# Kernel optimization log

Hardware: AMD Instinct MI355X
Metric: run time of the kernel (lower is better)

## Reference

```python
import jax, jax.numpy as jnp
import numpy as np

N_NODES = 50000
N_EDGES = 800000
IN_CH = 128
HID = 64
OUT_CH = 40


def _sage_conv(x, src, dst, W_l, b_l, W_r):
    # PyG SAGEConv (mean aggr): out = lin_l(mean_{j in N(i)} x_j) + lin_r(x_i)
    msgs = x[src]                                                # [E, d]
    summed = jax.ops.segment_sum(msgs, dst, num_segments=N_NODES)
    counts = jax.ops.segment_sum(jnp.ones((src.shape[0],), x.dtype), dst,
                                 num_segments=N_NODES)
    mean = summed / jnp.maximum(counts, 1.0)[:, None]            # [N, d]
    return mean @ W_l.T + b_l + x @ W_r.T


def setup_inputs() -> dict:
    key = jax.random.key(0)
    ks = jax.random.split(key, 8)
    x = jax.random.normal(ks[0], (N_NODES, IN_CH), dtype=jnp.float32)
    edge_index = jax.random.randint(ks[1], (2, N_EDGES), 0, N_NODES, dtype=jnp.int64)
    s1 = 1.0 / np.sqrt(IN_CH)
    s2 = 1.0 / np.sqrt(HID)
    W1_l = jax.random.uniform(ks[2], (HID, IN_CH), jnp.float32, -s1, s1)
    W1_r = jax.random.uniform(ks[3], (HID, IN_CH), jnp.float32, -s1, s1)
    b1 = jax.random.uniform(ks[4], (HID,), jnp.float32, -s1, s1)
    W2_l = jax.random.uniform(ks[5], (OUT_CH, HID), jnp.float32, -s2, s2)
    W2_r = jax.random.uniform(ks[6], (OUT_CH, HID), jnp.float32, -s2, s2)
    b2 = jax.random.uniform(ks[7], (OUT_CH,), jnp.float32, -s2, s2)
    return {"x": x, "edge_index": edge_index, "W1_l": W1_l, "b1": b1,
            "W1_r": W1_r, "W2_l": W2_l, "b2": b2, "W2_r": W2_r}


def reference(x, edge_index, W1_l, b1, W1_r, W2_l, b2, W2_r):
    src, dst = edge_index[0], edge_index[1]
    h = _sage_conv(x, src, dst, W1_l, b1, W1_r)
    h = jax.nn.relu(h)                       # dropout is identity in eval
    h = _sage_conv(h, src, dst, W2_l, b2, W2_r)
    return jax.nn.log_softmax(h, axis=-1)
```

## Files before the change

### kernel.cpp

```cpp
#include <hip/hip_runtime.h>

#define N_NODES 50000
#define N_EDGES 800000
#define IN_CH 128
#define HID 64
#define OUT_CH 40
#define BSHIFT 7
#define BNODES 128
#define NBUCKETS 391
#define NBLK 256
#define EPB 3125
#define NSEG (NBUCKETS * NBLK)
#define SCHUNK 1024
#define NSCANA ((NSEG + SCHUNK - 1) / SCHUNK)
#define MAXB 4096


typedef __attribute__((ext_vector_type(8))) short short8v;
typedef __attribute__((ext_vector_type(4))) float float4v;

__device__ __forceinline__ unsigned f2bf_u(float f) {
  unsigned u = __float_as_uint(f);
  return (u + 0x7FFF + ((u >> 16) & 1)) >> 16;
}
__device__ __forceinline__ ushort f2bf(float f) { return (ushort)f2bf_u(f); }
__device__ __forceinline__ float bf2f(ushort u) {
  return __uint_as_float(((unsigned)u) << 16);
}
__device__ __forceinline__ float bflo(unsigned u) {
  return __uint_as_float(u << 16);
}
__device__ __forceinline__ float bfhi(unsigned u) {
  return __uint_as_float(u & 0xFFFF0000u);
}

__global__ __launch_bounds__(256) void histB_kernel(const int* __restrict__ dst,
                                                    int* __restrict__ blkcnt) {
  __shared__ int h[NBUCKETS];
  for (int i = threadIdx.x; i < NBUCKETS; i += 256) h[i] = 0;
  __syncthreads();
  int blk = blockIdx.x;
  int e0 = blk * EPB, e1 = min(e0 + EPB, N_EDGES);
  for (int e = e0 + threadIdx.x; e < e1; e += 256)
    atomicAdd(&h[dst[e] >> BSHIFT], 1);
  __syncthreads();
  for (int i = threadIdx.x; i < NBUCKETS; i += 256)
    blkcnt[(i << 8) | blk] = h[i];
}

__global__ __launch_bounds__(256) void scanA_kernel(
    const int* __restrict__ blkcnt, int* __restrict__ segoff,
    int* __restrict__ asum) {
  __shared__ int s[256];
  int t = threadIdx.x;
  int idx0 = blockIdx.x * SCHUNK + t * 4;
  int v[4], tot = 0;
#pragma unroll
  for (int j = 0; j < 4; ++j) {
    int i = idx0 + j;
    v[j] = (i < NSEG) ? blkcnt[i] : 0;
    tot += v[j];
  }
  s[t] = tot;
  __syncthreads();
  for (int o = 1; o < 256; o <<= 1) {
    int u = (t >= o) ? s[t - o] : 0;
    __syncthreads();
    s[t] += u;
    __syncthreads();
  }
  int pre = s[t] - tot;
#pragma unroll
  for (int j = 0; j < 4; ++j) {
    int i = idx0 + j;
    if (i < NSEG) segoff[i] = pre;
    pre += v[j];
  }
  if (t == 255) asum[blockIdx.x] = s[255];
}

__global__ __launch_bounds__(256) void scanB_kernel(int* __restrict__ asum) {
  __shared__ int s[256];
  int t = threadIdx.x;
  int v = (t < NSCANA) ? asum[t] : 0;
  s[t] = v;
  __syncthreads();
  for (int o = 1; o < 256; o <<= 1) {
    int u = (t >= o) ? s[t - o] : 0;
    __syncthreads();
    s[t] += u;
    __syncthreads();
  }
  if (t < NSCANA) asum[t] = s[t] - v;
}

__global__ __launch_bounds__(256) void scanC_kernel(int* __restrict__ segoff,
                                                    const int* __restrict__ asum) {
  int add = asum[blockIdx.x];
  int idx0 = blockIdx.x * SCHUNK + threadIdx.x * 4;
#pragma unroll
  for (int j = 0; j < 4; ++j) {
    int i = idx0 + j;
    if (i < NSEG) segoff[i] += add;
  }
}

__global__ __launch_bounds__(256) void placeB_kernel(
    const int* __restrict__ src, const int* __restrict__ dst,
    const int* __restrict__ segoff, unsigned* __restrict__ pairbuf) {
  __shared__ int cur[NBUCKETS];
  int blk = blockIdx.x;
  for (int b = threadIdx.x; b < NBUCKETS; b += 256)
    cur[b] = segoff[(b << 8) | blk];
  __syncthreads();
  int e0 = blk * EPB, e1 = min(e0 + EPB, N_EDGES);
  for (int e = e0 + threadIdx.x; e < e1; e += 256) {
    int d = dst[e];
    int pos = atomicAdd(&cur[d >> BSHIFT], 1);
    pairbuf[pos] = ((unsigned)src[e] << BSHIFT) | (unsigned)(d & (BNODES - 1));
  }
}

__global__ __launch_bounds__(256) void placeC_kernel(
    const unsigned* __restrict__ pairbuf, const int* __restrict__ segoff,
    int* __restrict__ cnt, int* __restrict__ off, int* __restrict__ csr) {
  __shared__ int lcnt[BNODES];
  __shared__ int woff[BNODES];
  __shared__ int lcur[BNODES];
  __shared__ int sscan[256];
  __shared__ int slot[MAXB];
  int b = blockIdx.x;
  int start = segoff[b << 8];
  int end = (b == NBUCKETS - 1) ? N_EDGES : segoff[(b + 1) << 8];
  int n0 = b << BSHIFT;
  int nn = min(BNODES, N_NODES - n0);
  int len = end - start;
  for (int i = threadIdx.x; i < nn; i += 256) {
    lcnt[i] = 0;
    lcur[i] = 0;
  }
  __syncthreads();
  for (int p = start + threadIdx.x; p < end; p += 256)
    atomicAdd(&lcnt[pairbuf[p] & (BNODES - 1)], 1);
  __syncthreads();
  int v = (threadIdx.x < nn) ? lcnt[threadIdx.x] : 0;
  sscan[threadIdx.x] = v;
  __syncthreads();
  for (int o = 1; o < 256; o <<= 1) {
    int t2 = (threadIdx.x >= o) ? sscan[threadIdx.x - o] : 0;
    __syncthreads();
    sscan[threadIdx.x] += t2;
    __syncthreads();
  }
  if (threadIdx.x < nn) {
    woff[threadIdx.x] = sscan[threadIdx.x] - v;
    cnt[n0 + threadIdx.x] = v;
    off[n0 + threadIdx.x] = start + sscan[threadIdx.x] - v;
  }
  __syncthreads();
  if (len <= MAXB) {
    for (int p = start + threadIdx.x; p < end; p += 256) {
      unsigned e = pairbuf[p];
      int local = (int)(e & (BNODES - 1));
      int pos = woff[local] + atomicAdd(&lcur[local], 1);
      slot[pos] = (int)(e >> BSHIFT);
    }
    __syncthreads();
    for (int p = threadIdx.x; p < len; p += 256) csr[start + p] = slot[p];
  } else {
    for (int p = start + threadIdx.x; p < end; p += 256) {
      unsigned e = pairbuf[p];
      int local = (int)(e & (BNODES - 1));
      int pos = woff[local] + atomicAdd(&lcur[local], 1);
      csr[start + pos] = (int)(e >> BSHIFT);
    }
  }
}

__device__ __forceinline__ uint4 pack8(const float* p) {
  float4 a = *reinterpret_cast<const float4*>(p);
  float4 b = *reinterpret_cast<const float4*>(p + 4);
  uint4 r;
  r.x = f2bf_u(a.x) | (f2bf_u(a.y) << 16);
  r.y = f2bf_u(a.z) | (f2bf_u(a.w) << 16);
  r.z = f2bf_u(b.x) | (f2bf_u(b.y) << 16);
  r.w = f2bf_u(b.z) | (f2bf_u(b.w) << 16);
  return r;
}

__global__ __launch_bounds__(256) void xform1_kernel(
    const float* __restrict__ x, const float* __restrict__ W1l,
    const float* __restrict__ W1r, const float* __restrict__ b1,
    ushort* __restrict__ xwl, float* __restrict__ xwr) {
  __shared__ ushort sWl[64 * 128];
  __shared__ ushort sWr[64 * 128];
  __shared__ ushort sx[64 * 128];
  __shared__ float sb[64];

  int nblk = blockIdx.x * 64;
  for (int q = threadIdx.x; q < 1024; q += 256) {
    int row = q >> 4, c8 = (q & 15) << 3;
    int boff = row * 256 + (((c8 << 1)) ^ ((row & 15) << 4));
    int n = nblk + row;
    uint4 p = make_uint4(0, 0, 0, 0);
    if (n < N_NODES) p = pack8(x + (size_t)n * IN_CH + c8);
    *reinterpret_cast<uint4*>((char*)sx + boff) = p;
  }
  for (int q = threadIdx.x; q < 1024; q += 256) {
    int row = q >> 4, c8 = (q & 15) << 3;
    int boff = row * 256 + (((c8 << 1)) ^ ((row & 15) << 4));
    *reinterpret_cast<uint4*>((char*)sWl + boff) =
        pack8(W1l + row * IN_CH + c8);
    *reinterpret_cast<uint4*>((char*)sWr + boff) =
        pack8(W1r + row * IN_CH + c8);
  }
  if (threadIdx.x < 64) sb[threadIdx.x] = b1[threadIdx.x];
  __syncthreads();

  int wave = threadIdx.x >> 6, lane = threadIdx.x & 63;
  int nloc = lane & 15, g = lane >> 4;

  float4v accl[4], accr[4];
#pragma unroll
  for (int m = 0; m < 4; ++m) {
    accl[m] = (float4v){0.f, 0.f, 0.f, 0.f};
    accr[m] = (float4v){0.f, 0.f, 0.f, 0.f};
  }

  int xrow = wave * 16 + nloc;
#pragma unroll
  for (int kt = 0; kt < 4; ++kt) {
    int cb = kt * 64 + g * 16;
    short8v bx = *reinterpret_cast<const short8v*>(
        (char*)sx + xrow * 256 + (cb ^ ((xrow & 15) << 4)));
#pragma unroll
    for (int m = 0; m < 4; ++m) {
      int wrow = m * 16 + nloc;
      int so = wrow * 256 + (cb ^ ((wrow & 15) << 4));
      short8v al = *reinterpret_cast<const short8v*>((char*)sWl + so);
      short8v ar = *reinterpret_cast<const short8v*>((char*)sWr + so);
      accl[m] = __builtin_amdgcn_mfma_f32_16x16x32_bf16(al, bx, accl[m], 0, 0, 0);
      accr[m] = __builtin_amdgcn_mfma_f32_16x16x32_bf16(ar, bx, accr[m], 0, 0, 0);
    }
  }

  int n = nblk + wave * 16 + nloc;
  if (n < N_NODES) {
#pragma unroll
    for (int m = 0; m < 4; ++m) {
      int h0 = m * 16 + g * 4;
      uint2 pl;
      pl.x = f2bf_u(accl[m][0]) | (f2bf_u(accl[m][1]) << 16);
      pl.y = f2bf_u(accl[m][2]) | (f2bf_u(accl[m][3]) << 16);
      *reinterpret_cast<uint2*>(xwl + (size_t)n * HID + h0) = pl;
      float4 vr;
      vr.x = accr[m][0] + sb[h0 + 0];
      vr.y = accr[m][1] + sb[h0 + 1];
      vr.z = accr[m][2] + sb[h0 + 2];
      vr.w = accr[m][3] + sb[h0 + 3];
      *reinterpret_cast<float4*>(xwr + (size_t)n * HID + h0) = vr;
    }
  }
}

__global__ __launch_bounds__(256) void agg1_kernel(
    const ushort* __restrict__ xwl, const float* __restrict__ xwr,
    const int* __restrict__ cnt, const int* __restrict__ off,
    const int* __restrict__ csr, float* __restrict__ h1) {
  int wave = threadIdx.x >> 6, lane = threadIdx.x & 63;
  int n = blockIdx.x * 4 + wave;
  if (n >= N_NODES) return;

  int deg = cnt[n], base = off[n];
  int half = lane >> 5;
  int cp = lane & 31;
  float ax = 0.f, ay = 0.f;

  if (deg > 0) {
    int k = 0;
    for (; k + 16 <= deg; k += 16) {
      int e[8];
#pragma unroll
      for (int j = 0; j < 8; ++j) e[j] = csr[base + k + 2 * j + half];
      unsigned u[8];
#pragma unroll
      for (int j = 0; j < 8; ++j)
        u[j] = *reinterpret_cast<const unsigned*>(xwl + (size_t)e[j] * HID +
                                                  2 * cp);
#pragma unroll
      for (int j = 0; j < 8; ++j) {
        ax += bflo(u[j]);
        ay += bfhi(u[j]);
      }
    }
    if (k + 8 <= deg) {
      int e[4];
#pragma unroll
      for (int j = 0; j < 4; ++j) e[j] = csr[base + k + 2 * j + half];
      unsigned u[4];
#pragma unroll
      for (int j = 0; j < 4; ++j)
        u[j] = *reinterpret_cast<const unsigned*>(xwl + (size_t)e[j] * HID +
                                                  2 * cp);
#pragma unroll
      for (int j = 0; j < 4; ++j) {
        ax += bflo(u[j]);
        ay += bfhi(u[j]);
      }
      k += 8;
    }
    if (k < deg) {
#pragma unroll
      for (int j = 0; j < 4; ++j) {
        int idx = k + 2 * j + half;
        bool valid = idx < deg;
        int e = csr[base + (valid ? idx : 0)];
        unsigned u =
            *reinterpret_cast<const unsigned*>(xwl + (size_t)e * HID + 2 * cp);
        if (valid) {
          ax += bflo(u);
          ay += bfhi(u);
        }
      }
    }
    ax += __shfl_xor(ax, 32);
    ay += __shfl_xor(ay, 32);
  }

  float inv = 1.0f / fmaxf((float)deg, 1.0f);
  const float2 s =
      *reinterpret_cast<const float2*>(xwr + (size_t)n * HID + 2 * cp);
  float2 h;
  h.x = fmaxf(ax * inv + s.x, 0.f);
  h.y = fmaxf(ay * inv + s.y, 0.f);
  if (half == 0)
    *reinterpret_cast<float2*>(h1 + (size_t)n * HID + 2 * cp) = h;
}

__global__ __launch_bounds__(256) void xform2_kernel(
    const float* __restrict__ h1, const float* __restrict__ W2l,
    const float* __restrict__ W2r, const float* __restrict__ b2,
    ushort* __restrict__ hw2, float* __restrict__ self2) {
  __shared__ unsigned sWl[HID / 2][OUT_CH + 1];
  __shared__ unsigned sWr[HID / 2][OUT_CH + 1];
  __shared__ float sh[32][HID];
  for (int i = threadIdx.x; i < OUT_CH * (HID / 2); i += 256) {
    int o = i >> 5, c2 = i & 31;
    float a = W2l[o * HID + 2 * c2], b = W2l[o * HID + 2 * c2 + 1];
    sWl[c2][o] = (unsigned)f2bf(a) | ((unsigned)f2bf(b) << 16);
    float c = W2r[o * HID + 2 * c2], d = W2r[o * HID + 2 * c2 + 1];
    sWr[c2][o] = (unsigned)f2bf(c) | ((unsigned)f2bf(d) << 16);
  }
  int nblk = blockIdx.x * 32;
  for (int s = threadIdx.x; s < 32 * (HID / 4); s += 256) {
    int node = s >> 4, c4 = s & 15;
    int n = nblk + node;
    float4 v = make_float4(0.f, 0.f, 0.f, 0.f);
    if (n < N_NODES)
      v = *reinterpret_cast<const float4*>(h1 + (size_t)n * HID + c4 * 4);
    *reinterpret_cast<float4*>(&sh[node][c4 * 4]) = v;
  }
  __syncthreads();

  int wave = threadIdx.x >> 6, lane = threadIdx.x & 63;
  int n0 = nblk + wave * 8;
  if (n0 >= N_NODES || lane >= OUT_CH) return;
  float bias = b2[lane];

  float accl[8], accr[8];
#pragma unroll
  for (int i = 0; i < 8; ++i) {
    accl[i] = 0.f;
    accr[i] = bias;
  }
  const int nb = wave * 8;
  int nvalid = min(8, N_NODES - n0);
  for (int c = 0; c < HID; c += 4) {
    unsigned ul0 = sWl[(c >> 1) + 0][lane], ul1 = sWl[(c >> 1) + 1][lane];
    unsigned ur0 = sWr[(c >> 1) + 0][lane], ur1 = sWr[(c >> 1) + 1][lane];
    float wl0 = bflo(ul0), wl1 = bfhi(ul0), wl2 = bflo(ul1), wl3 = bfhi(ul1);
    float wr0 = bflo(ur0), wr1 = bfhi(ur0), wr2 = bflo(ur1), wr3 = bfhi(ur1);
#pragma unroll
    for (int i = 0; i < 8; ++i) {
      const float4 hv = *reinterpret_cast<const float4*>(&sh[nb + i][c]);
      accl[i] = fmaf(hv.x, wl0, accl[i]);
      accr[i] = fmaf(hv.x, wr0, accr[i]);
      accl[i] = fmaf(hv.y, wl1, accl[i]);
      accr[i] = fmaf(hv.y, wr1, accr[i]);
      accl[i] = fmaf(hv.z, wl2, accl[i]);
      accr[i] = fmaf(hv.z, wr2, accr[i]);
      accl[i] = fmaf(hv.w, wl3, accl[i]);
      accr[i] = fmaf(hv.w, wr3, accr[i]);
    }
  }
  for (int i = 0; i < nvalid; ++i) {
    hw2[(size_t)(n0 + i) * OUT_CH + lane] = f2bf(accl[i]);
    self2[(size_t)(n0 + i) * OUT_CH + lane] = accr[i];
  }
}

__global__ __launch_bounds__(256) void agg2_kernel(
    const ushort* __restrict__ hw2, const float* __restrict__ self2,
    const int* __restrict__ cnt, const int* __restrict__ off,
    const int* __restrict__ csr, float* __restrict__ out) {
  int wave = threadIdx.x >> 6, lane = threadIdx.x & 63;
  int n = blockIdx.x * 4 + wave;
  if (n >= N_NODES) return;

  int deg = cnt[n], base = off[n];
  float logit = -1e30f;
  if (lane < OUT_CH) {
    float acc = 0.f;
    int k = 0;
    for (; k + 16 <= deg; k += 16) {
      int e[16];
#pragma unroll
      for (int j = 0; j < 16; ++j) e[j] = csr[base + k + j];
      float v[16];
#pragma unroll
      for (int j = 0; j < 16; ++j)
        v[j] = bf2f(hw2[(size_t)e[j] * OUT_CH + lane]);
#pragma unroll
      for (int j = 0; j < 16; ++j) acc += v[j];
    }
    if (k + 8 <= deg) {
      int e[8];
#pragma unroll
      for (int j = 0; j < 8; ++j) e[j] = csr[base + k + j];
      float v[8];
#pragma unroll
      for (int j = 0; j < 8; ++j)
        v[j] = bf2f(hw2[(size_t)e[j] * OUT_CH + lane]);
#pragma unroll
      for (int j = 0; j < 8; ++j) acc += v[j];
      k += 8;
    }
    if (k < deg) {
#pragma unroll
      for (int i = 0; i < 8; ++i) {
        int kk = k + i;
        int s_ = csr[base + (kk < deg ? kk : k)];
        float v = bf2f(hw2[(size_t)s_ * OUT_CH + lane]);
        if (kk < deg) acc += v;
      }
    }
    logit = acc / fmaxf((float)deg, 1.0f) + self2[(size_t)n * OUT_CH + lane];
  }
  float m = logit;
  for (int o = 32; o; o >>= 1) m = fmaxf(m, __shfl_xor(m, o));
  float e = (lane < OUT_CH) ? expf(logit - m) : 0.f;
  float ssum = e;
  for (int o = 32; o; o >>= 1) ssum += __shfl_xor(ssum, o);
  float lse = logf(ssum);
  if (lane < OUT_CH) out[(size_t)n * OUT_CH + lane] = logit - m - lse;
}

extern "C" void kernel_launch(void* const* d_in, const int* in_sizes, int n_in,
                              void* d_out, int out_size, void* d_ws, size_t ws_size,
                              hipStream_t stream) {
  const float* x   = (const float*)d_in[0];
  const int*   ei  = (const int*)d_in[1];
  const float* W1l = (const float*)d_in[2];
  const float* b1  = (const float*)d_in[3];
  const float* W1r = (const float*)d_in[4];
  const float* W2l = (const float*)d_in[5];
  const float* b2  = (const float*)d_in[6];
  const float* W2r = (const float*)d_in[7];
  float* out = (float*)d_out;

  const int* src = ei;
  const int* dst = ei + N_EDGES;

  float* xwr        = (float*)d_ws;
  unsigned* pairbuf = (unsigned*)d_ws;
  float* self2 = xwr + (size_t)N_NODES * HID;
  float* h1    = self2 + (size_t)N_NODES * OUT_CH;
  ushort* xwl  = (ushort*)(h1 + (size_t)N_NODES * HID);
  ushort* hw2  = xwl + (size_t)N_NODES * HID;
  int* blkcnt = (int*)(hw2 + (size_t)N_NODES * OUT_CH);
  int* segoff = blkcnt + NSEG;
  int* asum   = segoff + NSEG;
  int* cnt    = asum + 256;
  int* off    = cnt + N_NODES;
  int* csr    = off + N_NODES;

  histB_kernel<<<NBLK, 256, 0, stream>>>(dst, blkcnt);
  scanA_kernel<<<NSCANA, 256, 0, stream>>>(blkcnt, segoff, asum);
  scanB_kernel<<<1, 256, 0, stream>>>(asum);
  scanC_kernel<<<NSCANA, 256, 0, stream>>>(segoff, asum);
  placeB_kernel<<<NBLK, 256, 0, stream>>>(src, dst, segoff, pairbuf);
  placeC_kernel<<<NBUCKETS, 256, 0, stream>>>(pairbuf, segoff, cnt, off, csr);

  xform1_kernel<<<(N_NODES + 63) / 64, 256, 0, stream>>>(x, W1l, W1r, b1, xwl,
                                                         xwr);
  agg1_kernel<<<(N_NODES + 3) / 4, 256, 0, stream>>>(xwl, xwr, cnt, off, csr,
                                                     h1);
  xform2_kernel<<<(N_NODES + 31) / 32, 256, 0, stream>>>(h1, W2l, W2r, b2, hw2,
                                                         self2);
  agg2_kernel<<<(N_NODES + 3) / 4, 256, 0, stream>>>(hw2, self2, cnt, off, csr,
                                                     out);
}
```

Baseline: 127.8 us.

## Merge layer-1 transform into histogram launch and fuse agg1 with xform2

```diff
diff --git a/kernel.cpp b/kernel.cpp
--- a/kernel.cpp
+++ b/kernel.cpp
@@ -14,6 +14,7 @@
 #define SCHUNK 1024
 #define NSCANA ((NSEG + SCHUNK - 1) / SCHUNK)
 #define MAXB 4096
+#define NXBLK 782
 
 
 typedef __attribute__((ext_vector_type(8))) short short8v;
@@ -34,18 +35,105 @@
   return __uint_as_float(u & 0xFFFF0000u);
 }
 
-__global__ __launch_bounds__(256) void histB_kernel(const int* __restrict__ dst,
-                                                    int* __restrict__ blkcnt) {
+__device__ __forceinline__ uint4 pack8(const float* p) {
+  float4 a = *reinterpret_cast<const float4*>(p);
+  float4 b = *reinterpret_cast<const float4*>(p + 4);
+  uint4 r;
+  r.x = f2bf_u(a.x) | (f2bf_u(a.y) << 16);
+  r.y = f2bf_u(a.z) | (f2bf_u(a.w) << 16);
+  r.z = f2bf_u(b.x) | (f2bf_u(b.y) << 16);
+  r.w = f2bf_u(b.z) | (f2bf_u(b.w) << 16);
+  return r;
+}
+
+__global__ __launch_bounds__(256) void histX_kernel(
+    const int* __restrict__ dst, int* __restrict__ blkcnt,
+    const float* __restrict__ x, const float* __restrict__ W1l,
+    const float* __restrict__ W1r, const float* __restrict__ b1,
+    ushort* __restrict__ xwl, float* __restrict__ xwr) {
   __shared__ int h[NBUCKETS];
-  for (int i = threadIdx.x; i < NBUCKETS; i += 256) h[i] = 0;
-  __syncthreads();
-  int blk = blockIdx.x;
-  int e0 = blk * EPB, e1 = min(e0 + EPB, N_EDGES);
-  for (int e = e0 + threadIdx.x; e < e1; e += 256)
-    atomicAdd(&h[dst[e] >> BSHIFT], 1);
-  __syncthreads();
-  for (int i = threadIdx.x; i < NBUCKETS; i += 256)
-    blkcnt[(i << 8) | blk] = h[i];
+  __shared__ ushort sWl[64 * 128];
+  __shared__ ushort sWr[64 * 128];
+  __shared__ ushort sx[64 * 128];
+  __shared__ float sb[64];
+
+  if (blockIdx.x < NBLK) {
+    for (int i = threadIdx.x; i < NBUCKETS; i += 256) h[i] = 0;
+    __syncthreads();
+    int blk = blockIdx.x;
+    int e0 = blk * EPB, e1 = min(e0 + EPB, N_EDGES);
+    for (int e = e0 + threadIdx.x; e < e1; e += 256)
+      atomicAdd(&h[dst[e] >> BSHIFT], 1);
+    __syncthreads();
+    for (int i = threadIdx.x; i < NBUCKETS; i += 256)
+      blkcnt[(i << 8) | blk] = h[i];
+    return;
+  }
+
+  int nblk = (blockIdx.x - NBLK) * 64;
+  for (int q = threadIdx.x; q < 1024; q += 256) {
+    int row = q >> 4, c8 = (q & 15) << 3;
+    int boff = row * 256 + (((c8 << 1)) ^ ((row & 15) << 4));
+    int n = nblk + row;
+    uint4 p = make_uint4(0, 0, 0, 0);
+    if (n < N_NODES) p = pack8(x + (size_t)n * IN_CH + c8);
+    *reinterpret_cast<uint4*>((char*)sx + boff) = p;
+  }
+  for (int q = threadIdx.x; q < 1024; q += 256) {
+    int row = q >> 4, c8 = (q & 15) << 3;
+    int boff = row * 256 + (((c8 << 1)) ^ ((row & 15) << 4));
+    *reinterpret_cast<uint4*>((char*)sWl + boff) =
+        pack8(W1l + row * IN_CH + c8);
+    *reinterpret_cast<uint4*>((char*)sWr + boff) =
+        pack8(W1r + row * IN_CH + c8);
+  }
+  if (threadIdx.x < 64) sb[threadIdx.x] = b1[threadIdx.x];
+  __syncthreads();
+
+  int wave = threadIdx.x >> 6, lane = threadIdx.x & 63;
+  int nloc = lane & 15, g = lane >> 4;
+
+  float4v accl[4], accr[4];
+#pragma unroll
+  for (int m = 0; m < 4; ++m) {
+    accl[m] = (float4v){0.f, 0.f, 0.f, 0.f};
+    accr[m] = (float4v){0.f, 0.f, 0.f, 0.f};
+  }
+
+  int xrow = wave * 16 + nloc;
+#pragma unroll
+  for (int kt = 0; kt < 4; ++kt) {
+    int cb = kt * 64 + g * 16;
+    short8v bx = *reinterpret_cast<const short8v*>(
+        (char*)sx + xrow * 256 + (cb ^ ((xrow & 15) << 4)));
+#pragma unroll
+    for (int m = 0; m < 4; ++m) {
+      int wrow = m * 16 + nloc;
+      int so = wrow * 256 + (cb ^ ((wrow & 15) << 4));
+      short8v al = *reinterpret_cast<const short8v*>((char*)sWl + so);
+      short8v ar = *reinterpret_cast<const short8v*>((char*)sWr + so);
+      accl[m] = __builtin_amdgcn_mfma_f32_16x16x32_bf16(al, bx, accl[m], 0, 0, 0);
+      accr[m] = __builtin_amdgcn_mfma_f32_16x16x32_bf16(ar, bx, accr[m], 0, 0, 0);
+    }
+  }
+
+  int n = nblk + wave * 16 + nloc;
+  if (n < N_NODES) {
+#pragma unroll
+    for (int m = 0; m < 4; ++m) {
+      int h0 = m * 16 + g * 4;
+      uint2 pl;
+      pl.x = f2bf_u(accl[m][0]) | (f2bf_u(accl[m][1]) << 16);
+      pl.y = f2bf_u(accl[m][2]) | (f2bf_u(accl[m][3]) << 16);
+      *reinterpret_cast<uint2*>(xwl + (size_t)n * HID + h0) = pl;
+      float4 vr;
+      vr.x = accr[m][0] + sb[h0 + 0];
+      vr.y = accr[m][1] + sb[h0 + 1];
+      vr.z = accr[m][2] + sb[h0 + 2];
+      vr.w = accr[m][3] + sb[h0 + 3];
+      *reinterpret_cast<float4*>(xwr + (size_t)n * HID + h0) = vr;
+    }
+  }
 }
 
 __global__ __launch_bounds__(256) void scanA_kernel(
@@ -177,169 +265,11 @@
   }
 }
 
-__device__ __forceinline__ uint4 pack8(const float* p) {
-  float4 a = *reinterpret_cast<const float4*>(p);
-  float4 b = *reinterpret_cast<const float4*>(p + 4);
-  uint4 r;
-  r.x = f2bf_u(a.x) | (f2bf_u(a.y) << 16);
-  r.y = f2bf_u(a.z) | (f2bf_u(a.w) << 16);
-  r.z = f2bf_u(b.x) | (f2bf_u(b.y) << 16);
-  r.w = f2bf_u(b.z) | (f2bf_u(b.w) << 16);
-  return r;
-}
-
-__global__ __launch_bounds__(256) void xform1_kernel(
-    const float* __restrict__ x, const float* __restrict__ W1l,
-    const float* __restrict__ W1r, const float* __restrict__ b1,
-    ushort* __restrict__ xwl, float* __restrict__ xwr) {
-  __shared__ ushort sWl[64 * 128];
-  __shared__ ushort sWr[64 * 128];
-  __shared__ ushort sx[64 * 128];
-  __shared__ float sb[64];
-
-  int nblk = blockIdx.x * 64;
-  for (int q = threadIdx.x; q < 1024; q += 256) {
-    int row = q >> 4, c8 = (q & 15) << 3;
-    int boff = row * 256 + (((c8 << 1)) ^ ((row & 15) << 4));
-    int n = nblk + row;
-    uint4 p = make_uint4(0, 0, 0, 0);
-    if (n < N_NODES) p = pack8(x + (size_t)n * IN_CH + c8);
-    *reinterpret_cast<uint4*>((char*)sx + boff) = p;
-  }
-  for (int q = threadIdx.x; q < 1024; q += 256) {
-    int row = q >> 4, c8 = (q & 15) << 3;
-    int boff = row * 256 + (((c8 << 1)) ^ ((row & 15) << 4));
-    *reinterpret_cast<uint4*>((char*)sWl + boff) =
-        pack8(W1l + row * IN_CH + c8);
-    *reinterpret_cast<uint4*>((char*)sWr + boff) =
-        pack8(W1r + row * IN_CH + c8);
-  }
-  if (threadIdx.x < 64) sb[threadIdx.x] = b1[threadIdx.x];
-  __syncthreads();
-
-  int wave = threadIdx.x >> 6, lane = threadIdx.x & 63;
-  int nloc = lane & 15, g = lane >> 4;
-
-  float4v accl[4], accr[4];
-#pragma unroll
-  for (int m = 0; m < 4; ++m) {
-    accl[m] = (float4v){0.f, 0.f, 0.f, 0.f};
-    accr[m] = (float4v){0.f, 0.f, 0.f, 0.f};
-  }
-
-  int xrow = wave * 16 + nloc;
-#pragma unroll
-  for (int kt = 0; kt < 4; ++kt) {
-    int cb = kt * 64 + g * 16;
-    short8v bx = *reinterpret_cast<const short8v*>(
-        (char*)sx + xrow * 256 + (cb ^ ((xrow & 15) << 4)));
-#pragma unroll
-    for (int m = 0; m < 4; ++m) {
-      int wrow = m * 16 + nloc;
-      int so = wrow * 256 + (cb ^ ((wrow & 15) << 4));
-      short8v al = *reinterpret_cast<const short8v*>((char*)sWl + so);
-      short8v ar = *reinterpret_cast<const short8v*>((char*)sWr + so);
-      accl[m] = __builtin_amdgcn_mfma_f32_16x16x32_bf16(al, bx, accl[m], 0, 0, 0);
-      accr[m] = __builtin_amdgcn_mfma_f32_16x16x32_bf16(ar, bx, accr[m], 0, 0, 0);
-    }
-  }
-
-  int n = nblk + wave * 16 + nloc;
-  if (n < N_NODES) {
-#pragma unroll
-    for (int m = 0; m < 4; ++m) {
-      int h0 = m * 16 + g * 4;
-      uint2 pl;
-      pl.x = f2bf_u(accl[m][0]) | (f2bf_u(accl[m][1]) << 16);
-      pl.y = f2bf_u(accl[m][2]) | (f2bf_u(accl[m][3]) << 16);
-      *reinterpret_cast<uint2*>(xwl + (size_t)n * HID + h0) = pl;
-      float4 vr;
-      vr.x = accr[m][0] + sb[h0 + 0];
-      vr.y = accr[m][1] + sb[h0 + 1];
-      vr.z = accr[m][2] + sb[h0 + 2];
-      vr.w = accr[m][3] + sb[h0 + 3];
-      *reinterpret_cast<float4*>(xwr + (size_t)n * HID + h0) = vr;
-    }
-  }
-}
-
-__global__ __launch_bounds__(256) void agg1_kernel(
+__global__ __launch_bounds__(256) void aggx2_kernel(
     const ushort* __restrict__ xwl, const float* __restrict__ xwr,
-    const int* __restrict__ cnt, const int* __restrict__ off,
-    const int* __restrict__ csr, float* __restrict__ h1) {
-  int wave = threadIdx.x >> 6, lane = threadIdx.x & 63;
-  int n = blockIdx.x * 4 + wave;
-  if (n >= N_NODES) return;
-
-  int deg = cnt[n], base = off[n];
-  int half = lane >> 5;
-  int cp = lane & 31;
-  float ax = 0.f, ay = 0.f;
-
-  if (deg > 0) {
-    int k = 0;
-    for (; k + 16 <= deg; k += 16) {
-      int e[8];
-#pragma unroll
-      for (int j = 0; j < 8; ++j) e[j] = csr[base + k + 2 * j + half];
-      unsigned u[8];
-#pragma unroll
-      for (int j = 0; j < 8; ++j)
-        u[j] = *reinterpret_cast<const unsigned*>(xwl + (size_t)e[j] * HID +
-                                                  2 * cp);
-#pragma unroll
-      for (int j = 0; j < 8; ++j) {
-        ax += bflo(u[j]);
-        ay += bfhi(u[j]);
-      }
-    }
-    if (k + 8 <= deg) {
-      int e[4];
-#pragma unroll
-      for (int j = 0; j < 4; ++j) e[j] = csr[base + k + 2 * j + half];
-      unsigned u[4];
-#pragma unroll
-      for (int j = 0; j < 4; ++j)
-        u[j] = *reinterpret_cast<const unsigned*>(xwl + (size_t)e[j] * HID +
-                                                  2 * cp);
-#pragma unroll
-      for (int j = 0; j < 4; ++j) {
-        ax += bflo(u[j]);
-        ay += bfhi(u[j]);
-      }
-      k += 8;
-    }
-    if (k < deg) {
-#pragma unroll
-      for (int j = 0; j < 4; ++j) {
-        int idx = k + 2 * j + half;
-        bool valid = idx < deg;
-        int e = csr[base + (valid ? idx : 0)];
-        unsigned u =
-            *reinterpret_cast<const unsigned*>(xwl + (size_t)e * HID + 2 * cp);
-        if (valid) {
-          ax += bflo(u);
-          ay += bfhi(u);
-        }
-      }
-    }
-    ax += __shfl_xor(ax, 32);
-    ay += __shfl_xor(ay, 32);
-  }
-
-  float inv = 1.0f / fmaxf((float)deg, 1.0f);
-  const float2 s =
-      *reinterpret_cast<const float2*>(xwr + (size_t)n * HID + 2 * cp);
-  float2 h;
-  h.x = fmaxf(ax * inv + s.x, 0.f);
-  h.y = fmaxf(ay * inv + s.y, 0.f);
-  if (half == 0)
-    *reinterpret_cast<float2*>(h1 + (size_t)n * HID + 2 * cp) = h;
-}
-
-__global__ __launch_bounds__(256) void xform2_kernel(
-    const float* __restrict__ h1, const float* __restrict__ W2l,
-    const float* __restrict__ W2r, const float* __restrict__ b2,
+    const float* __restrict__ W2l, const float* __restrict__ W2r,
+    const float* __restrict__ b2, const int* __restrict__ cnt,
+    const int* __restrict__ off, const int* __restrict__ csr,
     ushort* __restrict__ hw2, float* __restrict__ self2) {
   __shared__ unsigned sWl[HID / 2][OUT_CH + 1];
   __shared__ unsigned sWr[HID / 2][OUT_CH + 1];
@@ -351,22 +281,80 @@
     float c = W2r[o * HID + 2 * c2], d = W2r[o * HID + 2 * c2 + 1];
     sWr[c2][o] = (unsigned)f2bf(c) | ((unsigned)f2bf(d) << 16);
   }
-  int nblk = blockIdx.x * 32;
-  for (int s = threadIdx.x; s < 32 * (HID / 4); s += 256) {
-    int node = s >> 4, c4 = s & 15;
-    int n = nblk + node;
-    float4 v = make_float4(0.f, 0.f, 0.f, 0.f);
-    if (n < N_NODES)
-      v = *reinterpret_cast<const float4*>(h1 + (size_t)n * HID + c4 * 4);
-    *reinterpret_cast<float4*>(&sh[node][c4 * 4]) = v;
-  }
   __syncthreads();
 
   int wave = threadIdx.x >> 6, lane = threadIdx.x & 63;
-  int n0 = nblk + wave * 8;
-  if (n0 >= N_NODES || lane >= OUT_CH) return;
+  int n0 = blockIdx.x * 32 + wave * 8;
+  if (n0 >= N_NODES) return;
+  int half = lane >> 5;
+  int cp = lane & 31;
+
+  int nv = min(8, N_NODES - n0);
+  for (int i = 0; i < nv; ++i) {
+    int n = n0 + i;
+    int deg = cnt[n], base = off[n];
+    float ax = 0.f, ay = 0.f;
+    if (deg > 0) {
+      int k = 0;
+      for (; k + 16 <= deg; k += 16) {
+        int e[8];
+#pragma unroll
+        for (int j = 0; j < 8; ++j) e[j] = csr[base + k + 2 * j + half];
+        unsigned u[8];
+#pragma unroll
+        for (int j = 0; j < 8; ++j)
+          u[j] = *reinterpret_cast<const unsigned*>(xwl + (size_t)e[j] * HID +
+                                                    2 * cp);
+#pragma unroll
+        for (int j = 0; j < 8; ++j) {
+          ax += bflo(u[j]);
+          ay += bfhi(u[j]);
+        }
+      }
+      if (k + 8 <= deg) {
+        int e[4];
+#pragma unroll
+        for (int j = 0; j < 4; ++j) e[j] = csr[base + k + 2 * j + half];
+        unsigned u[4];
+#pragma unroll
+        for (int j = 0; j < 4; ++j)
+          u[j] = *reinterpret_cast<const unsigned*>(xwl + (size_t)e[j] * HID +
+                                                    2 * cp);
+#pragma unroll
+        for (int j = 0; j < 4; ++j) {
+          ax += bflo(u[j]);
+          ay += bfhi(u[j]);
+        }
+        k += 8;
+      }
+      if (k < deg) {
+#pragma unroll
+        for (int j = 0; j < 4; ++j) {
+          int idx = k + 2 * j + half;
+          bool valid = idx < deg;
+          int e = csr[base + (valid ? idx : 0)];
+          unsigned u = *reinterpret_cast<const unsigned*>(
+              xwl + (size_t)e * HID + 2 * cp);
+          if (valid) {
+            ax += bflo(u);
+            ay += bfhi(u);
+          }
+        }
+      }
+      ax += __shfl_xor(ax, 32);
+      ay += __shfl_xor(ay, 32);
+    }
+    float inv = 1.0f / fmaxf((float)deg, 1.0f);
+    const float2 s =
+        *reinterpret_cast<const float2*>(xwr + (size_t)n * HID + 2 * cp);
+    if (half == 0) {
+      sh[wave * 8 + i][2 * cp] = fmaxf(ax * inv + s.x, 0.f);
+      sh[wave * 8 + i][2 * cp + 1] = fmaxf(ay * inv + s.y, 0.f);
+    }
+  }
+
+  if (lane >= OUT_CH) return;
   float bias = b2[lane];
-
   float accl[8], accr[8];
 #pragma unroll
   for (int i = 0; i < 8; ++i) {
@@ -374,7 +362,6 @@
     accr[i] = bias;
   }
   const int nb = wave * 8;
-  int nvalid = min(8, N_NODES - n0);
   for (int c = 0; c < HID; c += 4) {
     unsigned ul0 = sWl[(c >> 1) + 0][lane], ul1 = sWl[(c >> 1) + 1][lane];
     unsigned ur0 = sWr[(c >> 1) + 0][lane], ur1 = sWr[(c >> 1) + 1][lane];
@@ -393,7 +380,7 @@
       accr[i] = fmaf(hv.w, wr3, accr[i]);
     }
   }
-  for (int i = 0; i < nvalid; ++i) {
+  for (int i = 0; i < nv; ++i) {
     hw2[(size_t)(n0 + i) * OUT_CH + lane] = f2bf(accl[i]);
     self2[(size_t)(n0 + i) * OUT_CH + lane] = accr[i];
   }
@@ -471,32 +458,28 @@
   const int* src = ei;
   const int* dst = ei + N_EDGES;
 
-  float* xwr        = (float*)d_ws;
-  unsigned* pairbuf = (unsigned*)d_ws;
+  float* xwr   = (float*)d_ws;
   float* self2 = xwr + (size_t)N_NODES * HID;
-  float* h1    = self2 + (size_t)N_NODES * OUT_CH;
-  ushort* xwl  = (ushort*)(h1 + (size_t)N_NODES * HID);
+  ushort* xwl  = (ushort*)(self2 + (size_t)N_NODES * OUT_CH);
   ushort* hw2  = xwl + (size_t)N_NODES * HID;
-  int* blkcnt = (int*)(hw2 + (size_t)N_NODES * OUT_CH);
+  unsigned* pairbuf = (unsigned*)(hw2 + (size_t)N_NODES * OUT_CH);
+  int* blkcnt = (int*)(pairbuf + N_EDGES);
   int* segoff = blkcnt + NSEG;
   int* asum   = segoff + NSEG;
   int* cnt    = asum + 256;
   int* off    = cnt + N_NODES;
   int* csr    = off + N_NODES;
 
-  histB_kernel<<<NBLK, 256, 0, stream>>>(dst, blkcnt);
+  histX_kernel<<<NBLK + NXBLK, 256, 0, stream>>>(dst, blkcnt, x, W1l, W1r, b1,
+                                                 xwl, xwr);
   scanA_kernel<<<NSCANA, 256, 0, stream>>>(blkcnt, segoff, asum);
   scanB_kernel<<<1, 256, 0, stream>>>(asum);
   scanC_kernel<<<NSCANA, 256, 0, stream>>>(segoff, asum);
   placeB_kernel<<<NBLK, 256, 0, stream>>>(src, dst, segoff, pairbuf);
   placeC_kernel<<<NBUCKETS, 256, 0, stream>>>(pairbuf, segoff, cnt, off, csr);
 
-  xform1_kernel<<<(N_NODES + 63) / 64, 256, 0, stream>>>(x, W1l, W1r, b1, xwl,
-                                                         xwr);
-  agg1_kernel<<<(N_NODES + 3) / 4, 256, 0, stream>>>(xwl, xwr, cnt, off, csr,
-                                                     h1);
-  xform2_kernel<<<(N_NODES + 31) / 32, 256, 0, stream>>>(h1, W2l, W2r, b2, hw2,
-                                                         self2);
+  aggx2_kernel<<<(N_NODES + 31) / 32, 256, 0, stream>>>(
+      xwl, xwr, W2l, W2r, b2, cnt, off, csr, hw2, self2);
   agg2_kernel<<<(N_NODES + 3) / 4, 256, 0, stream>>>(hw2, self2, cnt, off, csr,
                                                      out);
 }
```

Measured after the change: 135.2 us. 5.8% more time.
